# Optimization experiments

Measured on AMD Instinct MI355X. Metric: run time of the kernel, lower is better.

The kernel has to match this reference:

```python
import jax, jax.numpy as jnp
import numpy as np

NUM_HEADS = 4
KEY_DIM = 128


def rel_to_abs(rel):
    # rel: [B, heads, L, ww, 2*ww-1] -> [B, heads, L, ww, ww]
    B, heads, L, ww, dim = rel.shape
    flat = rel.reshape(B, heads, L, ww * (2 * ww - 1))[:, :, :, ww - 1:-1]
    return flat.reshape(B, heads, L, ww, 2 * (ww - 1))[..., :ww]


def relative_logits(pos_q, pos_emb_w, pos_emb_h):
    # pos_q: [B, hh, ww, heads, kd]
    # width logits
    q_w = jnp.transpose(pos_q, (0, 3, 1, 2, 4))           # [B, heads, hh, ww, kd]
    rel_w = jnp.einsum('bhxyd,dr->bhxyr', q_w, pos_emb_w)  # [B, heads, hh, ww, 2ww-1]
    rel_w = rel_to_abs(rel_w)                              # [B, heads, hh, ww, ww]
    # height logits
    q_h = jnp.transpose(pos_q, (0, 3, 2, 1, 4))           # [B, heads, ww, hh, kd]
    rel_h = jnp.einsum('bhyxd,dr->bhyxr', q_h, pos_emb_h)  # [B, heads, ww, hh, 2hh-1]
    rel_h = rel_to_abs(rel_h)                              # [B, heads, ww, hh, hh]
    rel_h = jnp.transpose(rel_h, (0, 1, 3, 2, 4))          # [B, heads, hh, ww, hh]
    # broadcast-add: [B, heads, hh, ww, hh, ww]
    return rel_w[:, :, :, :, None, :] + rel_h[:, :, :, :, :, None]


def setup_inputs() -> dict:
    key = jax.random.key(0)
    ks = jax.random.split(key, 7)
    B, H, W, C = 8, 32, 32, 512
    emb = NUM_HEADS * KEY_DIM
    stddev = KEY_DIM ** (-0.5)
    return {
        'x': jax.random.normal(ks[0], (B, H, W, C), jnp.float32),
        'Wq': jax.random.normal(ks[1], (C, emb), jnp.float32) * 0.02,
        'Wk': jax.random.normal(ks[2], (C, emb), jnp.float32) * 0.02,
        'Wv': jax.random.normal(ks[3], (C, emb), jnp.float32) * 0.02,
        'Wo': jax.random.normal(ks[4], (emb, emb), jnp.float32) * 0.02,
        'pos_emb_w': jax.random.normal(ks[5], (KEY_DIM, 2 * W - 1), jnp.float32) * stddev,
        'pos_emb_h': jax.random.normal(ks[6], (KEY_DIM, 2 * H - 1), jnp.float32) * stddev,
    }


def reference(x, Wq, Wk, Wv, Wo, pos_emb_w, pos_emb_h):
    B, hh, ww, C = x.shape
    heads, kd = NUM_HEADS, KEY_DIM
    L = hh * ww
    scale = 1.0 / jnp.sqrt(jnp.asarray(kd, x.dtype))

    q = (x @ Wq) * scale                                    # [B, hh, ww, heads*kd]
    attn_q = q.reshape(B, L, heads, kd).transpose(0, 2, 1, 3)   # [B, heads, L, kd]
    pos_q = q.reshape(B, hh, ww, heads, kd)
    k = (x @ Wk).reshape(B, L, heads, kd).transpose(0, 2, 3, 1)  # [B, heads, kd, L]
    v = (x @ Wv).reshape(B, L, heads, kd).transpose(0, 2, 1, 3)  # [B, heads, L, kd]

    scores = attn_q @ k                                      # [B, heads, L, L]
    pos = relative_logits(pos_q, pos_emb_w, pos_emb_h)        # [B, heads, hh, ww, hh, ww]
    scores = scores + pos.reshape(B, heads, L, L)
    attn = jax.nn.softmax(scores, axis=-1)

    out = attn @ v                                            # [B, heads, L, kd]
    out = out.transpose(0, 2, 1, 3).reshape(B, hh, ww, heads * kd)
    return out @ Wo
```

## Files before the change

kernel.cpp:

```cpp
#include <hip/hip_runtime.h>
#include <math.h>

typedef unsigned short u16;
typedef unsigned int u32;
typedef __bf16 bf16x8 __attribute__((ext_vector_type(8)));
typedef float f32x4 __attribute__((ext_vector_type(4)));

__device__ __forceinline__ u16 f2b(float f) {
  u32 u = __builtin_bit_cast(u32, f);
  u32 r = (u + 0x7FFFu + ((u >> 16) & 1u)) >> 16;
  return (u16)r;
}

__device__ __forceinline__ void glds16(const void* g, void* lds) {
  __builtin_amdgcn_global_load_lds(
      (const __attribute__((address_space(1))) void*)(void*)(const_cast<void*>(g)),
      (__attribute__((address_space(3))) void*)lds, 16, 0, 0);
}


__global__ __launch_bounds__(256) void castx(const float* __restrict__ x, u16* __restrict__ xb) {
  int idx = blockIdx.x * 256 + threadIdx.x;
  float4 v = ((const float4*)x)[idx];
  ushort4 o;
  o.x = f2b(v.x); o.y = f2b(v.y); o.z = f2b(v.z); o.w = f2b(v.w);
  ((ushort4*)xb)[idx] = o;
}

__global__ __launch_bounds__(256) void buildw(const float* __restrict__ Wq, const float* __restrict__ Wk,
                                              const float* __restrict__ Wv, const float* __restrict__ Wo,
                                              u16* __restrict__ WbigT, u16* __restrict__ WoT) {
  const float SCALE = 0.08838834764831845f;
  int row = blockIdx.x;
  int t = threadIdx.x;
  if (row < 512) {
    for (int k = t; k < 512; k += 256) WbigT[row*512 + k] = f2b(Wq[k*512 + row] * SCALE);
  } else if (row < 1024) {
    int n = row - 512;
    for (int k = t; k < 512; k += 256) WbigT[row*512 + k] = f2b(Wk[k*512 + n]);
  } else if (row < 1536) {
    int n = row - 1024;
    for (int k = t; k < 512; k += 256) WbigT[row*512 + k] = f2b(Wv[k*512 + n]);
  } else if (row < 1544) {
    int rr = row - 1536 + 2040;
    for (int k = t; k < 512; k += 256) WbigT[rr*512 + k] = 0;
  } else {
    int n = row - 1544;
    for (int k = t; k < 512; k += 256) WoT[n*512 + k] = f2b(Wo[k*512 + n]);
  }
}

__global__ __launch_bounds__(256) void wpe_kernel(const float* __restrict__ Wq, const float* __restrict__ pew,
                                                  const float* __restrict__ peh, u16* __restrict__ WbigT) {
  int k = blockIdx.x;
  int t = threadIdx.x;
  __shared__ float wrow[512];
  for (int j = t; j < 512; j += 256) wrow[j] = Wq[k*512 + j];
  __syncthreads();
  if (t < 252) {
    int h = t / 63, r = t - h*63;
    float aw = 0.f, ah = 0.f;
    for (int d = 0; d < 128; d++) {
      float qv = wrow[h*128 + d];
      aw += qv * pew[d*63 + r];
      ah += qv * peh[d*63 + r];
    }
    const float SCALE = 0.08838834764831845f;
    WbigT[(size_t)(1536 + t)*512 + k] = f2b(aw * SCALE);
    WbigT[(size_t)(1788 + t)*512 + k] = f2b(ah * SCALE);
  }
}

__global__ __launch_bounds__(512) void gemm256(
    const u16* __restrict__ A, const u16* __restrict__ Bt,
    u16* __restrict__ Qb, u16* __restrict__ Kb, u16* __restrict__ Vt,
    float* __restrict__ RELW, float* __restrict__ RELH)
{
  __shared__ char sm[131072];
  const int tid = threadIdx.x;
  const int w = tid >> 6, l = tid & 63, g = l >> 4, c = l & 15;
  const int bm = blockIdx.x, bn = blockIdx.y;
  const int wm = w >> 2, wn = w & 3;

  f32x4 acc[8][4];
#pragma unroll
  for (int i = 0; i < 8; i++)
#pragma unroll
    for (int j = 0; j < 4; j++) acc[i][j] = f32x4{0.f, 0.f, 0.f, 0.f};

  const char* Ab = (const char*)A;
  const char* Bb = (const char*)Bt;
  const int rsub = l >> 3;
  const int csw = (((l & 7) ^ rsub) << 4);

#define G_STAGE(kb, p)                                                                    \
  {                                                                                       \
    char* As_ = sm + (p)*65536;                                                           \
    char* Bs_ = As_ + 32768;                                                              \
    const int kbyte = (kb) * 128;                                                         \
    _Pragma("unroll")                                                                     \
    for (int i2 = 0; i2 < 4; i2++) {                                                      \
      const int row = i2*64 + w*8 + rsub;                                                 \
      glds16(Ab + (size_t)(bm*256 + row) * 1024 + kbyte + csw, As_ + i2*8192 + w*1024);   \
      glds16(Bb + (size_t)(bn*256 + row) * 1024 + kbyte + csw, Bs_ + i2*8192 + w*1024);   \
    }                                                                                     \
  }

  G_STAGE(0, 0);
  G_STAGE(1, 1);

#pragma unroll
  for (int kb = 0; kb < 8; kb++) {
    const int p = kb & 1;
    if (kb < 7) { asm volatile("s_waitcnt vmcnt(8)" ::: "memory"); }
    else        { asm volatile("s_waitcnt vmcnt(0)" ::: "memory"); }
    __builtin_amdgcn_s_barrier();
    const char* As_ = sm + p*65536;
    const char* Bs_ = As_ + 32768;
#pragma unroll
    for (int ks = 0; ks < 2; ks++) {
      const int koff = (ks*64 + g*16) ^ ((c & 7) << 4);
      bf16x8 af[8], bfr[4];
#pragma unroll
      for (int mf = 0; mf < 8; mf++)
        af[mf] = *(const bf16x8*)(As_ + (wm*128 + mf*16 + c)*128 + koff);
#pragma unroll
      for (int nf = 0; nf < 4; nf++)
        bfr[nf] = *(const bf16x8*)(Bs_ + (wn*64 + nf*16 + c)*128 + koff);
#pragma unroll
      for (int mf = 0; mf < 8; mf++)
#pragma unroll
        for (int nf = 0; nf < 4; nf++)
          acc[mf][nf] = __builtin_amdgcn_mfma_f32_16x16x32_bf16(af[mf], bfr[nf], acc[mf][nf], 0, 0, 0);
    }
    __builtin_amdgcn_s_barrier();
    if (kb < 6) G_STAGE(kb + 2, p);
  }
#undef G_STAGE

  const int b = bm >> 2;
  const int iBase = (bm & 3) * 256;

  if (bn < 4) {
    u16* dst0 = (bn < 2) ? Qb : Kb;
    const int bnn = bn & 1;
#pragma unroll
    for (int mf = 0; mf < 8; mf++) {
      const int lmb = wm*128 + mf*16 + g*4;
#pragma unroll
      for (int nf = 0; nf < 4; nf++) {
        const int ln = wn*64 + nf*16 + c;
#pragma unroll
        for (int r = 0; r < 4; r++) {
          const int lm = lmb + r;
          *(u16*)(sm + lm*512 + ((ln*2) ^ ((lm & 7) << 4))) = f2b(acc[mf][nf][r]);
        }
      }
    }
    __builtin_amdgcn_s_barrier();
#pragma unroll
    for (int it = 0; it < 16; it++) {
      const int gid = it*512 + tid;
      const int lm2 = gid >> 5, gsub = gid & 31;
      bf16x8 v = *(const bf16x8*)(sm + lm2*512 + ((gsub*16) ^ ((lm2 & 7) << 4)));
      const int h = bnn*2 + (gsub >> 4);
      const int d0 = (gsub & 15) * 8;
      *(bf16x8*)(dst0 + ((size_t)(b*4 + h)*1024 + iBase + lm2)*128 + d0) = v;
    }
  } else if (bn < 6) {
#pragma unroll
    for (int mf = 0; mf < 8; mf++) {
      const int lmb = wm*128 + mf*16 + g*4;
#pragma unroll
      for (int nf = 0; nf < 4; nf++) {
        const int ln = wn*64 + nf*16 + c;
        u32 w0, w1;
        asm("v_cvt_pk_bf16_f32 %0, %1, %2" : "=v"(w0) : "v"(acc[mf][nf][0]), "v"(acc[mf][nf][1]));
        asm("v_cvt_pk_bf16_f32 %0, %1, %2" : "=v"(w1) : "v"(acc[mf][nf][2]), "v"(acc[mf][nf][3]));
        uint2 pk; pk.x = w0; pk.y = w1;
        *(uint2*)(sm + ln*512 + ((lmb*2) ^ ((c & 7) << 4))) = pk;
      }
    }
    __builtin_amdgcn_s_barrier();
#pragma unroll
    for (int it = 0; it < 16; it++) {
      const int gid = it*512 + tid;
      const int ln2 = gid >> 5, gsub = gid & 31;
      bf16x8 v = *(const bf16x8*)(sm + ln2*512 + ((gsub*16) ^ ((ln2 & 7) << 4)));
      const int q2 = (bn - 4)*256 + ln2;
      const int h = q2 >> 7, d = q2 & 127;
      *(bf16x8*)(Vt + ((size_t)(b*4 + h)*128 + d)*1024 + iBase + gsub*8) = v;
    }
  } else {
#pragma unroll
    for (int mf = 0; mf < 8; mf++) {
      const int lmb = wm*128 + mf*16 + g*4;
#pragma unroll
      for (int nf = 0; nf < 4; nf++) {
        const int q = (bn - 6)*256 + wn*64 + nf*16 + c;
        if (q < 252) {
          const int h = q / 63, r2 = q - h*63;
#pragma unroll
          for (int r = 0; r < 4; r++)
            RELW[(size_t)((b*4 + h)*1024 + iBase + lmb + r)*64 + r2] = acc[mf][nf][r];
        } else if (q < 504) {
          const int qq = q - 252;
          const int h = qq / 63, r2 = qq - h*63;
#pragma unroll
          for (int r = 0; r < 4; r++)
            RELH[(size_t)((b*4 + h)*1024 + iBase + lmb + r)*64 + r2] = acc[mf][nf][r];
        }
      }
    }
  }
}

__global__ __launch_bounds__(256) void gemm_out(
    const u16* __restrict__ A, const u16* __restrict__ Bt, float* __restrict__ outF)
{
  __shared__ char sm[65536];
  const int tid = threadIdx.x;
  const int w = tid >> 6, l = tid & 63, g = l >> 4, c = l & 15;
  const int bm = blockIdx.x, bn = blockIdx.y;
  const int wm = (w >> 1) * 64, wn = (w & 1) * 64;

  f32x4 acc[4][4];
#pragma unroll
  for (int i = 0; i < 4; i++)
#pragma unroll
    for (int j = 0; j < 4; j++) acc[i][j] = f32x4{0.f, 0.f, 0.f, 0.f};

  const char* Ab = (const char*)A;
  const char* Bb = (const char*)Bt;
  const int rsub = l >> 3;
  const int csw = (((l & 7) ^ rsub) << 4);

#define G_STAGE(kb, p)                                                                    \
  {                                                                                       \
    char* As_ = sm + (p)*32768;                                                           \
    char* Bs_ = As_ + 16384;                                                              \
    const int kbyte = (kb) * 128;                                                         \
    _Pragma("unroll")                                                                     \
    for (int t = 0; t < 4; t++) {                                                         \
      const int row = (w*4 + t)*8 + rsub;                                                 \
      glds16(Ab + (size_t)(bm*128 + row) * 1024 + kbyte + csw, As_ + (w*4 + t)*1024);     \
      glds16(Bb + (size_t)(bn*128 + row) * 1024 + kbyte + csw, Bs_ + (w*4 + t)*1024);     \
    }                                                                                     \
  }

  G_STAGE(0, 0);
  G_STAGE(1, 1);

#pragma unroll
  for (int kb = 0; kb < 8; kb++) {
    const int p = kb & 1;
    if (kb < 7) { asm volatile("s_waitcnt vmcnt(8)" ::: "memory"); }
    else        { asm volatile("s_waitcnt vmcnt(0)" ::: "memory"); }
    __builtin_amdgcn_s_barrier();
    const char* As_ = sm + p*32768;
    const char* Bs_ = As_ + 16384;
#pragma unroll
    for (int ks = 0; ks < 2; ks++) {
      const int koff = (ks*64 + g*16) ^ ((c & 7) << 4);
      bf16x8 af[4], bfr[4];
#pragma unroll
      for (int mf = 0; mf < 4; mf++)
        af[mf] = *(const bf16x8*)(As_ + (wm + mf*16 + c)*128 + koff);
#pragma unroll
      for (int nf = 0; nf < 4; nf++)
        bfr[nf] = *(const bf16x8*)(Bs_ + (wn + nf*16 + c)*128 + koff);
#pragma unroll
      for (int mf = 0; mf < 4; mf++)
#pragma unroll
        for (int nf = 0; nf < 4; nf++)
          acc[mf][nf] = __builtin_amdgcn_mfma_f32_16x16x32_bf16(af[mf], bfr[nf], acc[mf][nf], 0, 0, 0);
    }
    __builtin_amdgcn_s_barrier();
    if (kb < 6) G_STAGE(kb + 2, p);
  }
#undef G_STAGE

#pragma unroll
  for (int mf = 0; mf < 4; mf++) {
#pragma unroll
    for (int nf = 0; nf < 4; nf++) {
      const int n = bn*128 + wn + nf*16 + c;
#pragma unroll
      for (int r = 0; r < 4; r++) {
        const int m = bm*128 + wm + mf*16 + g*4 + r;
        outF[(size_t)m*512 + n] = acc[mf][nf][r];
      }
    }
  }
}

__global__ __launch_bounds__(256) void attn_fused(
    const u16* __restrict__ Qb, const u16* __restrict__ Kb, const u16* __restrict__ Vt,
    const float* __restrict__ RELW, const float* __restrict__ RELH,
    u16* __restrict__ AO)
{
  __shared__ char sm[73728];
  char* const Pl = sm + 65536;
  const int tid = threadIdx.x;
  const int w = tid >> 6, l = tid & 63, g = l >> 4, c = l & 15;
  const int bh = blockIdx.x, qt = blockIdx.y;
  const int i0 = qt * 64;

  bf16x8 qf[4];
  {
    const char* qbase = (const char*)Qb + (size_t)(bh*1024 + i0 + w*16 + c) * 256;
#pragma unroll
    for (int s = 0; s < 4; s++) qf[s] = *(const bf16x8*)(qbase + s*64 + g*16);
  }

  const int i = i0 + w*16 + c;
  const int xi = i & 31, yi = i >> 5;
  const float* rw = RELW + ((size_t)(bh*1024 + i) << 6);
  const float* rhb = RELH + ((size_t)(bh*1024 + i) << 6) + (31 - yi);
  float xwh[2][4];
#pragma unroll
  for (int e = 0; e < 2; e++)
#pragma unroll
    for (int r = 0; r < 4; r++) xwh[e][r] = rw[e*16 + g*4 + r - xi + 31];

  f32x4 Oacc[8];
#pragma unroll
  for (int fd = 0; fd < 8; fd++) Oacc[fd] = f32x4{0.f, 0.f, 0.f, 0.f};
  float m_q = -INFINITY, l_q = 0.f;

#define A_STAGE(jt, p)                                                                     \
  {                                                                                        \
    char* Kt_ = sm + (p)*32768;                                                            \
    char* Vs_ = Kt_ + 16384;                                                               \
    const int j0b = (jt) * 64;                                                             \
    _Pragma("unroll")                                                                      \
    for (int t = 0; t < 4; t++) {                                                          \
      const int L = (w*4 + t)*1024 + l*16;                                                 \
      const int jr = L >> 8, jb = L & 255;                                                 \
      glds16((const char*)Kb + (size_t)(bh*1024 + j0b + jr) * 256 + (jb ^ ((jr & 7) << 4)),\
             Kt_ + L);                                                                     \
      const int dr = L >> 7, db = L & 127;                                                 \
      glds16((const char*)Vt + (size_t)(bh*128 + dr) * 2048 + j0b*2 + (db ^ ((dr & 7) << 4)),\
             Vs_ + L);                                                                     \
    }                                                                                      \
  }

  A_STAGE(0, 0);
  A_STAGE(1, 1);
  float yh0 = rhb[0], yh1 = rhb[1];

#pragma unroll 2
  for (int jt = 0; jt < 16; jt++) {
    const int p = jt & 1;
    if (jt < 15) { asm volatile("s_waitcnt vmcnt(8)" ::: "memory"); }
    else         { asm volatile("s_waitcnt vmcnt(0)" ::: "memory"); }
    __builtin_amdgcn_s_barrier();

    const char* Kt_ = sm + p*32768;
    const char* Vs_ = Kt_ + 16384;

    f32x4 acc[4];
#pragma unroll
    for (int fn = 0; fn < 4; fn++) acc[fn] = f32x4{0.f, 0.f, 0.f, 0.f};
    __builtin_amdgcn_s_setprio(1);
#pragma unroll
    for (int s = 0; s < 4; s++) {
      const int koff = (s*64 + g*16) ^ ((c & 7) << 4);
#pragma unroll
      for (int fn = 0; fn < 4; fn++) {
        bf16x8 kf = *(const bf16x8*)(Kt_ + (fn*16 + c)*256 + koff);
        acc[fn] = __builtin_amdgcn_mfma_f32_16x16x32_bf16(kf, qf[s], acc[fn], 0, 0, 0);
      }
    }
    __builtin_amdgcn_s_setprio(0);

#pragma unroll
    for (int fn = 0; fn < 4; fn++)
#pragma unroll
      for (int r = 0; r < 4; r++)
        acc[fn][r] += xwh[fn & 1][r] + ((fn >> 1) ? yh1 : yh0);

    float mx = fmaxf(fmaxf(fmaxf(acc[0][0], acc[0][1]), fmaxf(acc[0][2], acc[0][3])),
                     fmaxf(fmaxf(acc[1][0], acc[1][1]), fmaxf(acc[1][2], acc[1][3])));
    mx = fmaxf(mx, fmaxf(fmaxf(fmaxf(acc[2][0], acc[2][1]), fmaxf(acc[2][2], acc[2][3])),
                         fmaxf(fmaxf(acc[3][0], acc[3][1]), fmaxf(acc[3][2], acc[3][3]))));
    mx = fmaxf(mx, __shfl_xor(mx, 16));
    mx = fmaxf(mx, __shfl_xor(mx, 32));
    const float mnew = fmaxf(m_q, mx);
    const float scq = __expf(m_q - mnew);
    m_q = mnew;

    float pv[4][4];
    float ps = 0.f;
#pragma unroll
    for (int fn = 0; fn < 4; fn++) {
#pragma unroll
      for (int r = 0; r < 4; r++) {
        pv[fn][r] = __expf(acc[fn][r] - mnew);
        ps += pv[fn][r];
      }
    }
    ps += __shfl_xor(ps, 16);
    ps += __shfl_xor(ps, 32);
    l_q = l_q * scq + ps;

    float nyh0 = 0.f, nyh1 = 0.f;
    if (jt < 15) { nyh0 = rhb[(jt + 1)*2]; nyh1 = rhb[(jt + 1)*2 + 1]; }

    {
      char* pb = Pl + w*2048 + c*128;
      const int swz = (c & 7) << 4;
#pragma unroll
      for (int fn = 0; fn < 4; fn++) {
        u32 w0, w1;
        asm("v_cvt_pk_bf16_f32 %0, %1, %2" : "=v"(w0) : "v"(pv[fn][0]), "v"(pv[fn][1]));
        asm("v_cvt_pk_bf16_f32 %0, %1, %2" : "=v"(w1) : "v"(pv[fn][2]), "v"(pv[fn][3]));
        uint2 pk; pk.x = w0; pk.y = w1;
        *(uint2*)(pb + ((fn*32 + g*8) ^ swz)) = pk;
      }
    }

#pragma unroll
    for (int r = 0; r < 4; r++) {
      const float scr = __shfl(scq, g*4 + r, 16);
#pragma unroll
      for (int fd = 0; fd < 8; fd++) Oacc[fd][r] *= scr;
    }

    __builtin_amdgcn_s_setprio(1);
#pragma unroll
    for (int s = 0; s < 2; s++) {
      const int koff = (s*64 + g*16) ^ ((c & 7) << 4);
      bf16x8 pf = *(const bf16x8*)(Pl + w*2048 + c*128 + koff);
#pragma unroll
      for (int fd = 0; fd < 8; fd++) {
        bf16x8 vf = *(const bf16x8*)(Vs_ + (fd*16 + c)*128 + koff);
        Oacc[fd] = __builtin_amdgcn_mfma_f32_16x16x32_bf16(pf, vf, Oacc[fd], 0, 0, 0);
      }
    }
    __builtin_amdgcn_s_setprio(0);

    __builtin_amdgcn_s_barrier();
    if (jt < 14) A_STAGE(jt + 2, p);
    yh0 = nyh0; yh1 = nyh1;
  }

  const int b = bh >> 2, h = bh & 3;
#pragma unroll
  for (int r = 0; r < 4; r++) {
    const float lr = __shfl(l_q, g*4 + r, 16);
    const float linv = 1.0f / lr;
    const int io = i0 + w*16 + g*4 + r;
#pragma unroll
    for (int fd = 0; fd < 8; fd++) {
      AO[(size_t)(b*1024 + io)*512 + h*128 + fd*16 + c] = f2b(Oacc[fd][r] * linv);
    }
  }
#undef A_STAGE
}

extern "C" void kernel_launch(void* const* d_in, const int* in_sizes, int n_in,
                              void* d_out, int out_size, void* d_ws, size_t ws_size,
                              hipStream_t stream) {
  const float* x   = (const float*)d_in[0];
  const float* Wq  = (const float*)d_in[1];
  const float* Wk  = (const float*)d_in[2];
  const float* Wv  = (const float*)d_in[3];
  const float* Wo  = (const float*)d_in[4];
  const float* pew = (const float*)d_in[5];
  const float* peh = (const float*)d_in[6];

  char* ws = (char*)d_ws;
  u16* xb    = (u16*)ws;    ws += (size_t)8192*512*2;
  u16* WbigT = (u16*)ws;    ws += (size_t)2048*512*2;
  u16* WoT   = (u16*)ws;    ws += (size_t)512*512*2;
  u16* Qb    = (u16*)ws;    ws += (size_t)32*1024*128*2;
  u16* Kb    = (u16*)ws;    ws += (size_t)32*1024*128*2;
  u16* Vt    = (u16*)ws;    ws += (size_t)32*1024*128*2;
  float* RELW = (float*)ws; ws += (size_t)32*1024*64*4;
  float* RELH = (float*)ws; ws += (size_t)32*1024*64*4;
  u16* AO    = (u16*)ws;    ws += (size_t)8192*512*2;

  castx<<<4096, 256, 0, stream>>>(x, xb);
  buildw<<<2056, 256, 0, stream>>>(Wq, Wk, Wv, Wo, WbigT, WoT);
  wpe_kernel<<<512, 256, 0, stream>>>(Wq, pew, peh, WbigT);
  gemm256<<<dim3(32, 8), 512, 0, stream>>>(xb, WbigT, Qb, Kb, Vt, RELW, RELH);
  attn_fused<<<dim3(32, 16), 256, 0, stream>>>(Qb, Kb, Vt, RELW, RELH, AO);
  gemm_out<<<dim3(64, 4), 256, 0, stream>>>(AO, WoT, (float*)d_out);
}
```

Before: 97.63 us.

## Keep full-K weight tile resident in LDS, stream activations directly from global

Both projection GEMMs now load the entire K=512 slice of the weight tile into shared memory once, then read A fragments straight from global memory into registers instead of double-buffering A and B tiles through LDS. Tile shapes change (512x128 for QKV, 256x64 for the output GEMM), and the grids are adjusted to match. The aim is to remove per-k-step barriers and LDS staging of the activation matrix. In exchange, A loads go uncoalesced through the cache without prefetch pipelining, and the 128KB LDS footprint may prevent the requested two blocks per CU.

```diff
diff --git a/kernel.cpp b/kernel.cpp
--- a/kernel.cpp
+++ b/kernel.cpp
@@ -71,7 +71,7 @@
   }
 }
 
-__global__ __launch_bounds__(512) void gemm256(
+__global__ __launch_bounds__(512, 2) void gemm_qkv(
     const u16* __restrict__ A, const u16* __restrict__ Bt,
     u16* __restrict__ Qb, u16* __restrict__ Kb, u16* __restrict__ Vt,
     float* __restrict__ RELW, float* __restrict__ RELH)
@@ -80,135 +80,113 @@
   const int tid = threadIdx.x;
   const int w = tid >> 6, l = tid & 63, g = l >> 4, c = l & 15;
   const int bm = blockIdx.x, bn = blockIdx.y;
-  const int wm = w >> 2, wn = w & 3;
-
-  f32x4 acc[8][4];
-#pragma unroll
-  for (int i = 0; i < 8; i++)
-#pragma unroll
-    for (int j = 0; j < 4; j++) acc[i][j] = f32x4{0.f, 0.f, 0.f, 0.f};
-
-  const char* Ab = (const char*)A;
-  const char* Bb = (const char*)Bt;
-  const int rsub = l >> 3;
-  const int csw = (((l & 7) ^ rsub) << 4);
-
-#define G_STAGE(kb, p)                                                                    \
-  {                                                                                       \
-    char* As_ = sm + (p)*65536;                                                           \
-    char* Bs_ = As_ + 32768;                                                              \
-    const int kbyte = (kb) * 128;                                                         \
-    _Pragma("unroll")                                                                     \
-    for (int i2 = 0; i2 < 4; i2++) {                                                      \
-      const int row = i2*64 + w*8 + rsub;                                                 \
-      glds16(Ab + (size_t)(bm*256 + row) * 1024 + kbyte + csw, As_ + i2*8192 + w*1024);   \
-      glds16(Bb + (size_t)(bn*256 + row) * 1024 + kbyte + csw, Bs_ + i2*8192 + w*1024);   \
-    }                                                                                     \
-  }
-
-  G_STAGE(0, 0);
-  G_STAGE(1, 1);
-
-#pragma unroll
-  for (int kb = 0; kb < 8; kb++) {
-    const int p = kb & 1;
-    if (kb < 7) { asm volatile("s_waitcnt vmcnt(8)" ::: "memory"); }
-    else        { asm volatile("s_waitcnt vmcnt(0)" ::: "memory"); }
-    __builtin_amdgcn_s_barrier();
-    const char* As_ = sm + p*65536;
-    const char* Bs_ = As_ + 32768;
-#pragma unroll
-    for (int ks = 0; ks < 2; ks++) {
-      const int koff = (ks*64 + g*16) ^ ((c & 7) << 4);
-      bf16x8 af[8], bfr[4];
-#pragma unroll
-      for (int mf = 0; mf < 8; mf++)
-        af[mf] = *(const bf16x8*)(As_ + (wm*128 + mf*16 + c)*128 + koff);
-#pragma unroll
-      for (int nf = 0; nf < 4; nf++)
-        bfr[nf] = *(const bf16x8*)(Bs_ + (wn*64 + nf*16 + c)*128 + koff);
-#pragma unroll
-      for (int mf = 0; mf < 8; mf++)
-#pragma unroll
-        for (int nf = 0; nf < 4; nf++)
-          acc[mf][nf] = __builtin_amdgcn_mfma_f32_16x16x32_bf16(af[mf], bfr[nf], acc[mf][nf], 0, 0, 0);
-    }
-    __builtin_amdgcn_s_barrier();
-    if (kb < 6) G_STAGE(kb + 2, p);
-  }
-#undef G_STAGE
-
-  const int b = bm >> 2;
-  const int iBase = (bm & 3) * 256;
-
-  if (bn < 4) {
-    u16* dst0 = (bn < 2) ? Qb : Kb;
-    const int bnn = bn & 1;
-#pragma unroll
-    for (int mf = 0; mf < 8; mf++) {
-      const int lmb = wm*128 + mf*16 + g*4;
-#pragma unroll
-      for (int nf = 0; nf < 4; nf++) {
-        const int ln = wn*64 + nf*16 + c;
+
+  {
+    const char* Bb = (const char*)Bt;
+#pragma unroll
+    for (int u = 0; u < 16; u++) {
+      const int n = u*8 + w;
+      glds16(Bb + (size_t)(bn*128 + n)*1024 + ((l*16) ^ ((n & 7) << 4)),
+             sm + u*8192 + w*1024);
+    }
+    asm volatile("s_waitcnt vmcnt(0)" ::: "memory");
+    __builtin_amdgcn_s_barrier();
+  }
+
+  f32x4 acc[4][8];
+#pragma unroll
+  for (int i = 0; i < 4; i++)
+#pragma unroll
+    for (int j = 0; j < 8; j++) acc[i][j] = f32x4{0.f, 0.f, 0.f, 0.f};
+
+  const char* Ab = (const char*)A + (size_t)(bm*512 + w*64 + c)*1024 + g*16;
+
+#pragma unroll 4
+  for (int kb = 0; kb < 16; kb++) {
+    bf16x8 af[4];
+#pragma unroll
+    for (int mf = 0; mf < 4; mf++)
+      af[mf] = *(const bf16x8*)(Ab + mf*16384 + kb*64);
+    bf16x8 bfr[8];
+#pragma unroll
+    for (int nf = 0; nf < 8; nf++)
+      bfr[nf] = *(const bf16x8*)(sm + (nf*16 + c)*1024 + ((kb*64 + g*16) ^ ((c & 7) << 4)));
+#pragma unroll
+    for (int mf = 0; mf < 4; mf++)
+#pragma unroll
+      for (int nf = 0; nf < 8; nf++)
+        acc[mf][nf] = __builtin_amdgcn_mfma_f32_16x16x32_bf16(af[mf], bfr[nf], acc[mf][nf], 0, 0, 0);
+  }
+
+  __builtin_amdgcn_s_barrier();
+
+  const int b = bm >> 1;
+  const int iB = (bm & 1) * 512;
+
+  if (bn < 8) {
+    u16* dst0 = (bn < 4) ? Qb : Kb;
+    const int h = bn & 3;
+#pragma unroll
+    for (int mf = 0; mf < 4; mf++) {
+#pragma unroll
+      for (int nf = 0; nf < 8; nf++) {
+        const int d = nf*16 + c;
 #pragma unroll
         for (int r = 0; r < 4; r++) {
-          const int lm = lmb + r;
-          *(u16*)(sm + lm*512 + ((ln*2) ^ ((lm & 7) << 4))) = f2b(acc[mf][nf][r]);
+          const int ml = w*64 + mf*16 + g*4 + r;
+          *(u16*)(sm + ml*256 + ((d*2) ^ ((ml & 7) << 4))) = f2b(acc[mf][nf][r]);
         }
       }
     }
     __builtin_amdgcn_s_barrier();
 #pragma unroll
     for (int it = 0; it < 16; it++) {
-      const int gid = it*512 + tid;
-      const int lm2 = gid >> 5, gsub = gid & 31;
-      bf16x8 v = *(const bf16x8*)(sm + lm2*512 + ((gsub*16) ^ ((lm2 & 7) << 4)));
-      const int h = bnn*2 + (gsub >> 4);
-      const int d0 = (gsub & 15) * 8;
-      *(bf16x8*)(dst0 + ((size_t)(b*4 + h)*1024 + iBase + lm2)*128 + d0) = v;
-    }
-  } else if (bn < 6) {
-#pragma unroll
-    for (int mf = 0; mf < 8; mf++) {
-      const int lmb = wm*128 + mf*16 + g*4;
-#pragma unroll
-      for (int nf = 0; nf < 4; nf++) {
-        const int ln = wn*64 + nf*16 + c;
+      const int chunk = it*512 + tid;
+      const int ml = chunk >> 4, d0 = (chunk & 15) * 8;
+      bf16x8 v = *(const bf16x8*)(sm + ml*256 + ((d0*2) ^ ((ml & 7) << 4)));
+      *(bf16x8*)(dst0 + ((size_t)(b*4 + h)*1024 + iB + ml)*128 + d0) = v;
+    }
+  } else if (bn < 12) {
+    const int h = bn - 8;
+#pragma unroll
+    for (int mf = 0; mf < 4; mf++) {
+      const int mlb = w*64 + mf*16 + g*4;
+#pragma unroll
+      for (int nf = 0; nf < 8; nf++) {
+        const int d = nf*16 + c;
         u32 w0, w1;
         asm("v_cvt_pk_bf16_f32 %0, %1, %2" : "=v"(w0) : "v"(acc[mf][nf][0]), "v"(acc[mf][nf][1]));
         asm("v_cvt_pk_bf16_f32 %0, %1, %2" : "=v"(w1) : "v"(acc[mf][nf][2]), "v"(acc[mf][nf][3]));
         uint2 pk; pk.x = w0; pk.y = w1;
-        *(uint2*)(sm + ln*512 + ((lmb*2) ^ ((c & 7) << 4))) = pk;
+        *(uint2*)(sm + d*1024 + ((mlb*2) ^ ((d & 7) << 4))) = pk;
       }
     }
     __builtin_amdgcn_s_barrier();
 #pragma unroll
     for (int it = 0; it < 16; it++) {
-      const int gid = it*512 + tid;
-      const int ln2 = gid >> 5, gsub = gid & 31;
-      bf16x8 v = *(const bf16x8*)(sm + ln2*512 + ((gsub*16) ^ ((ln2 & 7) << 4)));
-      const int q2 = (bn - 4)*256 + ln2;
-      const int h = q2 >> 7, d = q2 & 127;
-      *(bf16x8*)(Vt + ((size_t)(b*4 + h)*128 + d)*1024 + iBase + gsub*8) = v;
+      const int chunk = it*512 + tid;
+      const int d = chunk >> 6, m0 = (chunk & 63) * 8;
+      bf16x8 v = *(const bf16x8*)(sm + d*1024 + ((m0*2) ^ ((d & 7) << 4)));
+      *(bf16x8*)(Vt + ((size_t)(b*4 + h)*128 + d)*1024 + iB + m0) = v;
     }
   } else {
 #pragma unroll
-    for (int mf = 0; mf < 8; mf++) {
-      const int lmb = wm*128 + mf*16 + g*4;
-#pragma unroll
-      for (int nf = 0; nf < 4; nf++) {
-        const int q = (bn - 6)*256 + wn*64 + nf*16 + c;
+    for (int mf = 0; mf < 4; mf++) {
+      const int mlb = w*64 + mf*16 + g*4;
+#pragma unroll
+      for (int nf = 0; nf < 8; nf++) {
+        const int q = (bn - 12)*128 + nf*16 + c;
         if (q < 252) {
           const int h = q / 63, r2 = q - h*63;
 #pragma unroll
           for (int r = 0; r < 4; r++)
-            RELW[(size_t)((b*4 + h)*1024 + iBase + lmb + r)*64 + r2] = acc[mf][nf][r];
+            RELW[(size_t)((b*4 + h)*1024 + iB + mlb + r)*64 + r2] = acc[mf][nf][r];
         } else if (q < 504) {
           const int qq = q - 252;
           const int h = qq / 63, r2 = qq - h*63;
 #pragma unroll
           for (int r = 0; r < 4; r++)
-            RELH[(size_t)((b*4 + h)*1024 + iBase + lmb + r)*64 + r2] = acc[mf][nf][r];
+            RELH[(size_t)((b*4 + h)*1024 + iB + mlb + r)*64 + r2] = acc[mf][nf][r];
         }
       }
     }
@@ -222,7 +200,18 @@
   const int tid = threadIdx.x;
   const int w = tid >> 6, l = tid & 63, g = l >> 4, c = l & 15;
   const int bm = blockIdx.x, bn = blockIdx.y;
-  const int wm = (w >> 1) * 64, wn = (w & 1) * 64;
+
+  {
+    const char* Bb = (const char*)Bt;
+#pragma unroll
+    for (int u = 0; u < 16; u++) {
+      const int n = u*4 + w;
+      glds16(Bb + (size_t)(bn*64 + n)*1024 + ((l*16) ^ ((n & 7) << 4)),
+             sm + u*4096 + w*1024);
+    }
+    asm volatile("s_waitcnt vmcnt(0)" ::: "memory");
+    __builtin_amdgcn_s_barrier();
+  }
 
   f32x4 acc[4][4];
 #pragma unroll
@@ -230,64 +219,33 @@
 #pragma unroll
     for (int j = 0; j < 4; j++) acc[i][j] = f32x4{0.f, 0.f, 0.f, 0.f};
 
-  const char* Ab = (const char*)A;
-  const char* Bb = (const char*)Bt;
-  const int rsub = l >> 3;
-  const int csw = (((l & 7) ^ rsub) << 4);
-
-#define G_STAGE(kb, p)                                                                    \
-  {                                                                                       \
-    char* As_ = sm + (p)*32768;                                                           \
-    char* Bs_ = As_ + 16384;                                                              \
-    const int kbyte = (kb) * 128;                                                         \
-    _Pragma("unroll")                                                                     \
-    for (int t = 0; t < 4; t++) {                                                         \
-      const int row = (w*4 + t)*8 + rsub;                                                 \
-      glds16(Ab + (size_t)(bm*128 + row) * 1024 + kbyte + csw, As_ + (w*4 + t)*1024);     \
-      glds16(Bb + (size_t)(bn*128 + row) * 1024 + kbyte + csw, Bs_ + (w*4 + t)*1024);     \
-    }                                                                                     \
-  }
-
-  G_STAGE(0, 0);
-  G_STAGE(1, 1);
-
-#pragma unroll
-  for (int kb = 0; kb < 8; kb++) {
-    const int p = kb & 1;
-    if (kb < 7) { asm volatile("s_waitcnt vmcnt(8)" ::: "memory"); }
-    else        { asm volatile("s_waitcnt vmcnt(0)" ::: "memory"); }
-    __builtin_amdgcn_s_barrier();
-    const char* As_ = sm + p*32768;
-    const char* Bs_ = As_ + 16384;
-#pragma unroll
-    for (int ks = 0; ks < 2; ks++) {
-      const int koff = (ks*64 + g*16) ^ ((c & 7) << 4);
-      bf16x8 af[4], bfr[4];
-#pragma unroll
-      for (int mf = 0; mf < 4; mf++)
-        af[mf] = *(const bf16x8*)(As_ + (wm + mf*16 + c)*128 + koff);
+  const char* Ab = (const char*)A + (size_t)(bm*256 + w*64 + c)*1024 + g*16;
+
+#pragma unroll 4
+  for (int kb = 0; kb < 16; kb++) {
+    bf16x8 af[4];
+#pragma unroll
+    for (int mf = 0; mf < 4; mf++)
+      af[mf] = *(const bf16x8*)(Ab + mf*16384 + kb*64);
+    bf16x8 bfr[4];
+#pragma unroll
+    for (int nf = 0; nf < 4; nf++)
+      bfr[nf] = *(const bf16x8*)(sm + (nf*16 + c)*1024 + ((kb*64 + g*16) ^ ((c & 7) << 4)));
+#pragma unroll
+    for (int mf = 0; mf < 4; mf++)
 #pragma unroll
       for (int nf = 0; nf < 4; nf++)
-        bfr[nf] = *(const bf16x8*)(Bs_ + (wn + nf*16 + c)*128 + koff);
-#pragma unroll
-      for (int mf = 0; mf < 4; mf++)
-#pragma unroll
-        for (int nf = 0; nf < 4; nf++)
-          acc[mf][nf] = __builtin_amdgcn_mfma_f32_16x16x32_bf16(af[mf], bfr[nf], acc[mf][nf], 0, 0, 0);
-    }
-    __builtin_amdgcn_s_barrier();
-    if (kb < 6) G_STAGE(kb + 2, p);
-  }
-#undef G_STAGE
+        acc[mf][nf] = __builtin_amdgcn_mfma_f32_16x16x32_bf16(af[mf], bfr[nf], acc[mf][nf], 0, 0, 0);
+  }
 
 #pragma unroll
   for (int mf = 0; mf < 4; mf++) {
 #pragma unroll
     for (int nf = 0; nf < 4; nf++) {
-      const int n = bn*128 + wn + nf*16 + c;
+      const int n = bn*64 + nf*16 + c;
 #pragma unroll
       for (int r = 0; r < 4; r++) {
-        const int m = bm*128 + wm + mf*16 + g*4 + r;
+        const int m = bm*256 + w*64 + mf*16 + g*4 + r;
         outF[(size_t)m*512 + n] = acc[mf][nf][r];
       }
     }
@@ -484,7 +442,7 @@
   castx<<<4096, 256, 0, stream>>>(x, xb);
   buildw<<<2056, 256, 0, stream>>>(Wq, Wk, Wv, Wo, WbigT, WoT);
   wpe_kernel<<<512, 256, 0, stream>>>(Wq, pew, peh, WbigT);
-  gemm256<<<dim3(32, 8), 512, 0, stream>>>(xb, WbigT, Qb, Kb, Vt, RELW, RELH);
+  gemm_qkv<<<dim3(16, 16), 512, 0, stream>>>(xb, WbigT, Qb, Kb, Vt, RELW, RELH);
   attn_fused<<<dim3(32, 16), 256, 0, stream>>>(Qb, Kb, Vt, RELW, RELH, AO);
-  gemm_out<<<dim3(64, 4), 256, 0, stream>>>(AO, WoT, (float*)d_out);
-}
+  gemm_out<<<dim3(32, 8), 256, 0, stream>>>(AO, WoT, (float*)d_out);
+}
```

Result: slower. 111.3 us (+14.0%).

## Split attention over key halves with merge kernel, V read directly from global

Applied to the files above, without the earlier changes.

The attention kernel now splits each query tile's key range into two halves (flash-decoding style), doubling the grid to 1024 blocks. Each block writes unnormalized partial outputs plus its running max and sum. A new merge kernel combines the two halves in place, and gemm_out reads the merged result in the per-head layout. V is no longer staged in LDS but loaded straight from global memory, shrinking shared memory so that four blocks can fit per CU. The aim is better occupancy and CU utilisation, at the cost of an extra kernel launch, extra global traffic for the partials, and bf16 rounding of the unnormalized partial outputs.

```diff
diff --git a/kernel.cpp b/kernel.cpp
--- a/kernel.cpp
+++ b/kernel.cpp
@@ -10,6 +10,11 @@
   u32 u = __builtin_bit_cast(u32, f);
   u32 r = (u + 0x7FFFu + ((u >> 16) & 1u)) >> 16;
   return (u16)r;
+}
+
+__device__ __forceinline__ float b2f(u16 b) {
+  u32 u = ((u32)b) << 16;
+  return __builtin_bit_cast(float, u);
 }
 
 __device__ __forceinline__ void glds16(const void* g, void* lds) {
@@ -215,96 +220,18 @@
   }
 }
 
-__global__ __launch_bounds__(256) void gemm_out(
-    const u16* __restrict__ A, const u16* __restrict__ Bt, float* __restrict__ outF)
+__global__ __launch_bounds__(256, 4) void attn_split(
+    const u16* __restrict__ Qb, const u16* __restrict__ Kb, const u16* __restrict__ Vt,
+    const float* __restrict__ RELW, const float* __restrict__ RELH,
+    u16* __restrict__ Opart, float2* __restrict__ ML)
 {
-  __shared__ char sm[65536];
+  __shared__ char sm[40960];
+  char* const Pl = sm + 32768;
   const int tid = threadIdx.x;
   const int w = tid >> 6, l = tid & 63, g = l >> 4, c = l & 15;
-  const int bm = blockIdx.x, bn = blockIdx.y;
-  const int wm = (w >> 1) * 64, wn = (w & 1) * 64;
-
-  f32x4 acc[4][4];
-#pragma unroll
-  for (int i = 0; i < 4; i++)
-#pragma unroll
-    for (int j = 0; j < 4; j++) acc[i][j] = f32x4{0.f, 0.f, 0.f, 0.f};
-
-  const char* Ab = (const char*)A;
-  const char* Bb = (const char*)Bt;
-  const int rsub = l >> 3;
-  const int csw = (((l & 7) ^ rsub) << 4);
-
-#define G_STAGE(kb, p)                                                                    \
-  {                                                                                       \
-    char* As_ = sm + (p)*32768;                                                           \
-    char* Bs_ = As_ + 16384;                                                              \
-    const int kbyte = (kb) * 128;                                                         \
-    _Pragma("unroll")                                                                     \
-    for (int t = 0; t < 4; t++) {                                                         \
-      const int row = (w*4 + t)*8 + rsub;                                                 \
-      glds16(Ab + (size_t)(bm*128 + row) * 1024 + kbyte + csw, As_ + (w*4 + t)*1024);     \
-      glds16(Bb + (size_t)(bn*128 + row) * 1024 + kbyte + csw, Bs_ + (w*4 + t)*1024);     \
-    }                                                                                     \
-  }
-
-  G_STAGE(0, 0);
-  G_STAGE(1, 1);
-
-#pragma unroll
-  for (int kb = 0; kb < 8; kb++) {
-    const int p = kb & 1;
-    if (kb < 7) { asm volatile("s_waitcnt vmcnt(8)" ::: "memory"); }
-    else        { asm volatile("s_waitcnt vmcnt(0)" ::: "memory"); }
-    __builtin_amdgcn_s_barrier();
-    const char* As_ = sm + p*32768;
-    const char* Bs_ = As_ + 16384;
-#pragma unroll
-    for (int ks = 0; ks < 2; ks++) {
-      const int koff = (ks*64 + g*16) ^ ((c & 7) << 4);
-      bf16x8 af[4], bfr[4];
-#pragma unroll
-      for (int mf = 0; mf < 4; mf++)
-        af[mf] = *(const bf16x8*)(As_ + (wm + mf*16 + c)*128 + koff);
-#pragma unroll
-      for (int nf = 0; nf < 4; nf++)
-        bfr[nf] = *(const bf16x8*)(Bs_ + (wn + nf*16 + c)*128 + koff);
-#pragma unroll
-      for (int mf = 0; mf < 4; mf++)
-#pragma unroll
-        for (int nf = 0; nf < 4; nf++)
-          acc[mf][nf] = __builtin_amdgcn_mfma_f32_16x16x32_bf16(af[mf], bfr[nf], acc[mf][nf], 0, 0, 0);
-    }
-    __builtin_amdgcn_s_barrier();
-    if (kb < 6) G_STAGE(kb + 2, p);
-  }
-#undef G_STAGE
-
-#pragma unroll
-  for (int mf = 0; mf < 4; mf++) {
-#pragma unroll
-    for (int nf = 0; nf < 4; nf++) {
-      const int n = bn*128 + wn + nf*16 + c;
-#pragma unroll
-      for (int r = 0; r < 4; r++) {
-        const int m = bm*128 + wm + mf*16 + g*4 + r;
-        outF[(size_t)m*512 + n] = acc[mf][nf][r];
-      }
-    }
-  }
-}
-
-__global__ __launch_bounds__(256) void attn_fused(
-    const u16* __restrict__ Qb, const u16* __restrict__ Kb, const u16* __restrict__ Vt,
-    const float* __restrict__ RELW, const float* __restrict__ RELH,
-    u16* __restrict__ AO)
-{
-  __shared__ char sm[73728];
-  char* const Pl = sm + 65536;
-  const int tid = threadIdx.x;
-  const int w = tid >> 6, l = tid & 63, g = l >> 4, c = l & 15;
-  const int bh = blockIdx.x, qt = blockIdx.y;
-  const int i0 = qt * 64;
+  const int bh = blockIdx.x;
+  const int qt = blockIdx.y & 15, half = blockIdx.y >> 4;
+  const int i0 = qt * 64, jt0 = half * 8;
 
   bf16x8 qf[4];
   {
@@ -323,15 +250,11 @@
 #pragma unroll
     for (int r = 0; r < 4; r++) xwh[e][r] = rw[e*16 + g*4 + r - xi + 31];
 
-  f32x4 Oacc[8];
-#pragma unroll
-  for (int fd = 0; fd < 8; fd++) Oacc[fd] = f32x4{0.f, 0.f, 0.f, 0.f};
-  float m_q = -INFINITY, l_q = 0.f;
-
-#define A_STAGE(jt, p)                                                                     \
+  float yh0 = rhb[jt0*2], yh1 = rhb[jt0*2 + 1];
+
+#define K_STAGE(jt, p)                                                                     \
   {                                                                                        \
-    char* Kt_ = sm + (p)*32768;                                                            \
-    char* Vs_ = Kt_ + 16384;                                                               \
+    char* Kt_ = sm + (p)*16384;                                                            \
     const int j0b = (jt) * 64;                                                             \
     _Pragma("unroll")                                                                      \
     for (int t = 0; t < 4; t++) {                                                          \
@@ -339,25 +262,27 @@
       const int jr = L >> 8, jb = L & 255;                                                 \
       glds16((const char*)Kb + (size_t)(bh*1024 + j0b + jr) * 256 + (jb ^ ((jr & 7) << 4)),\
              Kt_ + L);                                                                     \
-      const int dr = L >> 7, db = L & 127;                                                 \
-      glds16((const char*)Vt + (size_t)(bh*128 + dr) * 2048 + j0b*2 + (db ^ ((dr & 7) << 4)),\
-             Vs_ + L);                                                                     \
     }                                                                                      \
   }
 
-  A_STAGE(0, 0);
-  A_STAGE(1, 1);
-  float yh0 = rhb[0], yh1 = rhb[1];
-
-#pragma unroll 2
-  for (int jt = 0; jt < 16; jt++) {
-    const int p = jt & 1;
-    if (jt < 15) { asm volatile("s_waitcnt vmcnt(8)" ::: "memory"); }
-    else         { asm volatile("s_waitcnt vmcnt(0)" ::: "memory"); }
-    __builtin_amdgcn_s_barrier();
-
-    const char* Kt_ = sm + p*32768;
-    const char* Vs_ = Kt_ + 16384;
+  K_STAGE(jt0, 0);
+  K_STAGE(jt0 + 1, 1);
+
+  f32x4 Oacc[8];
+#pragma unroll
+  for (int fd = 0; fd < 8; fd++) Oacc[fd] = f32x4{0.f, 0.f, 0.f, 0.f};
+  float m_q = -INFINITY, l_q = 0.f;
+
+#pragma unroll
+  for (int jj = 0; jj < 8; jj++) {
+    const int jt = jt0 + jj;
+    const int p = jj & 1;
+    if (jj == 0)      { asm volatile("s_waitcnt vmcnt(4)" ::: "memory"); }
+    else if (jj == 7) { asm volatile("s_waitcnt vmcnt(2)" ::: "memory"); }
+    else              { asm volatile("s_waitcnt vmcnt(6)" ::: "memory"); }
+    __builtin_amdgcn_s_barrier();
+
+    const char* Kt_ = sm + p*16384;
 
     f32x4 acc[4];
 #pragma unroll
@@ -405,7 +330,7 @@
     l_q = l_q * scq + ps;
 
     float nyh0 = 0.f, nyh1 = 0.f;
-    if (jt < 15) { nyh0 = rhb[(jt + 1)*2]; nyh1 = rhb[(jt + 1)*2 + 1]; }
+    if (jj < 7) { nyh0 = rhb[(jt + 1)*2]; nyh1 = rhb[(jt + 1)*2 + 1]; }
 
     {
       char* pb = Pl + w*2048 + c*128;
@@ -432,31 +357,152 @@
     for (int s = 0; s < 2; s++) {
       const int koff = (s*64 + g*16) ^ ((c & 7) << 4);
       bf16x8 pf = *(const bf16x8*)(Pl + w*2048 + c*128 + koff);
-#pragma unroll
-      for (int fd = 0; fd < 8; fd++) {
-        bf16x8 vf = *(const bf16x8*)(Vs_ + (fd*16 + c)*128 + koff);
-        Oacc[fd] = __builtin_amdgcn_mfma_f32_16x16x32_bf16(pf, vf, Oacc[fd], 0, 0, 0);
+      const size_t vbase = (size_t)(bh*128 + c)*1024 + jt*64 + s*32 + g*8;
+#pragma unroll
+      for (int fb = 0; fb < 2; fb++) {
+        bf16x8 vfa[4];
+#pragma unroll
+        for (int q4 = 0; q4 < 4; q4++)
+          vfa[q4] = *(const bf16x8*)(Vt + vbase + (size_t)(fb*4 + q4)*16*1024);
+#pragma unroll
+        for (int q4 = 0; q4 < 4; q4++)
+          Oacc[fb*4 + q4] = __builtin_amdgcn_mfma_f32_16x16x32_bf16(pf, vfa[q4], Oacc[fb*4 + q4], 0, 0, 0);
       }
     }
     __builtin_amdgcn_s_setprio(0);
 
     __builtin_amdgcn_s_barrier();
-    if (jt < 14) A_STAGE(jt + 2, p);
+    if (jj < 6) K_STAGE(jt + 2, p);
     yh0 = nyh0; yh1 = nyh1;
   }
-
-  const int b = bh >> 2, h = bh & 3;
-#pragma unroll
-  for (int r = 0; r < 4; r++) {
-    const float lr = __shfl(l_q, g*4 + r, 16);
-    const float linv = 1.0f / lr;
-    const int io = i0 + w*16 + g*4 + r;
-#pragma unroll
-    for (int fd = 0; fd < 8; fd++) {
-      AO[(size_t)(b*1024 + io)*512 + h*128 + fd*16 + c] = f2b(Oacc[fd][r] * linv);
-    }
-  }
-#undef A_STAGE
+#undef K_STAGE
+
+  const size_t rbase = (size_t)(half*32 + bh)*1024;
+#pragma unroll
+  for (int fd = 0; fd < 8; fd++) {
+#pragma unroll
+    for (int r = 0; r < 4; r++) {
+      const int io = i0 + w*16 + g*4 + r;
+      Opart[(rbase + io)*128 + fd*16 + c] = f2b(Oacc[fd][r]);
+    }
+  }
+  if (l < 16) {
+    float2 s2; s2.x = m_q; s2.y = l_q;
+    ML[rbase + i0 + w*16 + l] = s2;
+  }
+}
+
+__global__ __launch_bounds__(256) void attn_merge(
+    u16* __restrict__ Opart, const float2* __restrict__ ML)
+{
+  const int bh = blockIdx.x, qb = blockIdx.y;
+  const int t = threadIdx.x;
+  const int row = t >> 3, dg = t & 7;
+  const int i = qb*32 + row;
+  const size_t r0 = (size_t)bh*1024 + i;
+  const size_t r1 = (size_t)(32 + bh)*1024 + i;
+  const float2 ml0 = ML[r0], ml1 = ML[r1];
+  const float m = fmaxf(ml0.x, ml1.x);
+  const float w0 = __expf(ml0.x - m), w1 = __expf(ml1.x - m);
+  const float linv = 1.0f / (ml0.y*w0 + ml1.y*w1);
+  u16* p0 = Opart + r0*128 + dg*16;
+  const u16* p1 = Opart + r1*128 + dg*16;
+#pragma unroll
+  for (int hlf = 0; hlf < 2; hlf++) {
+    bf16x8 a = *(const bf16x8*)(p0 + hlf*8);
+    bf16x8 b = *(const bf16x8*)(p1 + hlf*8);
+    u16 outv[8];
+#pragma unroll
+    for (int e = 0; e < 8; e++) {
+      float va = b2f(((const u16*)&a)[e]);
+      float vb = b2f(((const u16*)&b)[e]);
+      outv[e] = f2b((va*w0 + vb*w1) * linv);
+    }
+    *(bf16x8*)(p0 + hlf*8) = *(const bf16x8*)outv;
+  }
+}
+
+__global__ __launch_bounds__(256) void gemm_out(
+    const u16* __restrict__ A, const u16* __restrict__ Bt, float* __restrict__ outF)
+{
+  __shared__ char sm[65536];
+  const int tid = threadIdx.x;
+  const int w = tid >> 6, l = tid & 63, g = l >> 4, c = l & 15;
+  const int bm = blockIdx.x, bn = blockIdx.y;
+  const int wm = (w >> 1) * 64, wn = (w & 1) * 64;
+
+  f32x4 acc[4][4];
+#pragma unroll
+  for (int i = 0; i < 4; i++)
+#pragma unroll
+    for (int j = 0; j < 4; j++) acc[i][j] = f32x4{0.f, 0.f, 0.f, 0.f};
+
+  const char* Ab = (const char*)A;
+  const char* Bb = (const char*)Bt;
+  const int rsub = l >> 3;
+  const int csw = (((l & 7) ^ rsub) << 4);
+  const int b_ = bm >> 3;
+  const int iT = (bm & 7) * 128;
+
+#define G_STAGE(kb, p)                                                                    \
+  {                                                                                       \
+    char* As_ = sm + (p)*32768;                                                           \
+    char* Bs_ = As_ + 16384;                                                              \
+    const int h_ = (kb) >> 1;                                                             \
+    const int dof = ((kb) & 1) * 128;                                                     \
+    _Pragma("unroll")                                                                     \
+    for (int t = 0; t < 4; t++) {                                                         \
+      const int row = (w*4 + t)*8 + rsub;                                                 \
+      glds16(Ab + (size_t)((b_*4 + h_)*1024 + iT + row) * 256 + dof + csw,                \
+             As_ + (w*4 + t)*1024);                                                       \
+      glds16(Bb + (size_t)(bn*128 + row) * 1024 + (kb)*128 + csw, Bs_ + (w*4 + t)*1024);  \
+    }                                                                                     \
+  }
+
+  G_STAGE(0, 0);
+  G_STAGE(1, 1);
+
+#pragma unroll
+  for (int kb = 0; kb < 8; kb++) {
+    const int p = kb & 1;
+    if (kb < 7) { asm volatile("s_waitcnt vmcnt(8)" ::: "memory"); }
+    else        { asm volatile("s_waitcnt vmcnt(0)" ::: "memory"); }
+    __builtin_amdgcn_s_barrier();
+    const char* As_ = sm + p*32768;
+    const char* Bs_ = As_ + 16384;
+#pragma unroll
+    for (int ks = 0; ks < 2; ks++) {
+      const int koff = (ks*64 + g*16) ^ ((c & 7) << 4);
+      bf16x8 af[4], bfr[4];
+#pragma unroll
+      for (int mf = 0; mf < 4; mf++)
+        af[mf] = *(const bf16x8*)(As_ + (wm + mf*16 + c)*128 + koff);
+#pragma unroll
+      for (int nf = 0; nf < 4; nf++)
+        bfr[nf] = *(const bf16x8*)(Bs_ + (wn + nf*16 + c)*128 + koff);
+#pragma unroll
+      for (int mf = 0; mf < 4; mf++)
+#pragma unroll
+        for (int nf = 0; nf < 4; nf++)
+          acc[mf][nf] = __builtin_amdgcn_mfma_f32_16x16x32_bf16(af[mf], bfr[nf], acc[mf][nf], 0, 0, 0);
+    }
+    __builtin_amdgcn_s_barrier();
+    if (kb < 6) G_STAGE(kb + 2, p);
+  }
+#undef G_STAGE
+
+#pragma unroll
+  for (int mf = 0; mf < 4; mf++) {
+#pragma unroll
+    for (int nf = 0; nf < 4; nf++) {
+      const int n = bn*128 + wn + nf*16 + c;
+#pragma unroll
+      for (int r = 0; r < 4; r++) {
+        const int m = bm*128 + wm + mf*16 + g*4 + r;
+        outF[(size_t)m*512 + n] = acc[mf][nf][r];
+      }
+    }
+  }
 }
 
 extern "C" void kernel_launch(void* const* d_in, const int* in_sizes, int n_in,
@@ -479,12 +525,14 @@
   u16* Vt    = (u16*)ws;    ws += (size_t)32*1024*128*2;
   float* RELW = (float*)ws; ws += (size_t)32*1024*64*4;
   float* RELH = (float*)ws; ws += (size_t)32*1024*64*4;
-  u16* AO    = (u16*)ws;    ws += (size_t)8192*512*2;
+  u16* Opart = (u16*)ws;    ws += (size_t)2*32*1024*128*2;
+  float2* MLb = (float2*)ws; ws += (size_t)2*32*1024*8;
 
   castx<<<4096, 256, 0, stream>>>(x, xb);
   buildw<<<2056, 256, 0, stream>>>(Wq, Wk, Wv, Wo, WbigT, WoT);
   wpe_kernel<<<512, 256, 0, stream>>>(Wq, pew, peh, WbigT);
   gemm256<<<dim3(32, 8), 512, 0, stream>>>(xb, WbigT, Qb, Kb, Vt, RELW, RELH);
-  attn_fused<<<dim3(32, 16), 256, 0, stream>>>(Qb, Kb, Vt, RELW, RELH, AO);
-  gemm_out<<<dim3(64, 4), 256, 0, stream>>>(AO, WoT, (float*)d_out);
-}
+  attn_split<<<dim3(32, 32), 256, 0, stream>>>(Qb, Kb, Vt, RELW, RELH, Opart, MLb);
+  attn_merge<<<dim3(32, 32), 256, 0, stream>>>(Opart, MLb);
+  gemm_out<<<dim3(64, 4), 256, 0, stream>>>(Opart, WoT, (float*)d_out);
+}
```

After: 147.0 us. 50.5% more time.
